# Kernel optimization log

Hardware: AMD Instinct MI355X
Metric: run time of the kernel (lower is better)

The kernel has to match this reference:

```python
import jax, jax.numpy as jnp
import numpy as np

N, S, F, D = 4096, 128, 128, 256  # batch, memory slots, feat_dim, dim_h_o
EPS = 1e-8  # torch CosineSimilarity eps


def _xavier(key, shape):
    fan_out, fan_in = shape
    std = float(np.sqrt(2.0 / (fan_in + fan_out)))
    return jax.random.normal(key, shape, dtype=jnp.float32) * std


def setup_inputs() -> dict:
    key = jax.random.key(0)
    ks = jax.random.split(key, 10)
    return {
        "h_o_prev": jax.random.normal(ks[0], (N, D), dtype=jnp.float32),
        "C": jax.random.normal(ks[1], (N, S, F), dtype=jnp.float32),
        "Wk": _xavier(ks[2], (F, D)), "bk": jnp.zeros((F,), jnp.float32),
        "Wb": _xavier(ks[3], (1, D)), "bb": jnp.zeros((1,), jnp.float32),
        "We": _xavier(ks[4], (F, D)), "be": jnp.zeros((F,), jnp.float32),
        "Wv": _xavier(ks[5], (F, D)), "bv": jnp.zeros((F,), jnp.float32),
        "Wih": _xavier(ks[6], (3 * D, F)), "Whh": _xavier(ks[7], (3 * D, D)),
        "bih": jnp.zeros((3 * D,), jnp.float32), "bhh": jnp.zeros((3 * D,), jnp.float32),
    }


def reference(h_o_prev, C, Wk, bk, Wb, bb, We, be, Wv, bv, Wih, Whh, bih, bhh):
    # --- Attention (content addressing) ---
    k = h_o_prev @ Wk.T + bk                              # [N, F]
    beta_pre = h_o_prev @ Wb.T + bb                       # [N, 1]
    # clamp-split softplus trick in source == softplus(x) + 1
    beta = jax.nn.softplus(beta_pre) + 1.0                # [N, 1]
    C_norm = jnp.maximum(jnp.linalg.norm(C, axis=2), EPS)           # [N, S]
    k_norm = jnp.maximum(jnp.linalg.norm(k, axis=1, keepdims=True), EPS)  # [N, 1]
    s = jnp.einsum("nsf,nf->ns", C, k) / (C_norm * k_norm)          # cosine sim [N, S]
    w = jax.nn.softmax(s * beta, axis=1)                  # [N, S]
    # --- Read memory ---
    r = jnp.einsum("ns,nsf->nf", w, C)                    # [N, F]
    # --- GRU cell update (torch GRUCell semantics) ---
    gi = r @ Wih.T + bih                                  # [N, 3D]
    gh = h_o_prev @ Whh.T + bhh                           # [N, 3D]
    i_r, i_z, i_n = jnp.split(gi, 3, axis=1)
    h_r, h_z, h_n = jnp.split(gh, 3, axis=1)
    rg = jax.nn.sigmoid(i_r + h_r)
    z = jax.nn.sigmoid(i_z + h_z)
    n = jnp.tanh(i_n + rg * h_n)
    h_o = (1.0 - z) * n + z * h_o_prev                    # [N, D]
    # --- Write memory (erase + add, outer products) ---
    e = jax.nn.sigmoid(h_o @ We.T + be)                   # [N, F]
    v = h_o @ Wv.T + bv                                   # [N, F]
    w2 = w[:, :, None]                                    # [N, S, 1]
    C_new = C * (1.0 - w2 * e[:, None, :]) + w2 * v[:, None, :]
    return h_o, C_new, k, r
```

## Files before the change

### kernel.cpp

```cpp
#include <hip/hip_runtime.h>
#include <hip/hip_bf16.h>
#include <cstddef>
#include <cstdint>

constexpr int Nn = 4096;
constexpr int Ss = 128;
constexpr int Ff = 128;
constexpr int Dd = 256;
constexpr float EPSV = 1e-8f;

constexpr size_t HO_OFF = 0;
constexpr size_t C_OFF  = (size_t)Nn * Dd;
constexpr size_t K_OFF  = C_OFF + (size_t)Nn * Ss * Ff;
constexpr size_t R_OFF  = K_OFF + (size_t)Nn * Ff;

typedef __attribute__((ext_vector_type(4))) float f4v;
typedef __attribute__((ext_vector_type(8))) short bh8;
typedef __attribute__((ext_vector_type(4))) short bh4;

constexpr int WK_O  = 0;
constexpr int WHH_O = 32768;
constexpr int WIH_O = 229376;
constexpr int WEV_O = 327680;
constexpr int W_TOT = 393216;

__device__ __forceinline__ float sigmf(float x) { return 1.0f / (1.0f + __expf(-x)); }

__device__ __forceinline__ short f2bf(float x) {
    __hip_bfloat16 h = __float2bfloat16(x);
    return *reinterpret_cast<short*>(&h);
}

__device__ __forceinline__ int swzH(int row, int kb) { return row * 512 + (kb ^ ((row & 7) << 4)); }
__device__ __forceinline__ int swzR(int row, int kb) { return row * 256 + (kb ^ ((row & 7) << 4)); }

__device__ __forceinline__ f4v mfma16(bh8 a, bh8 b, f4v c) {
    return __builtin_amdgcn_mfma_f32_16x16x32_bf16(a, b, c, 0, 0, 0);
}

__global__ __launch_bounds__(256) void prep_weights(
    const float* __restrict__ Wk, const float* __restrict__ Whh,
    const float* __restrict__ Wih, const float* __restrict__ We,
    const float* __restrict__ Wv, short* __restrict__ out)
{
    int id = blockIdx.x * 256 + threadIdx.x;
    float v;
    if      (id < WHH_O) v = Wk[id - WK_O];
    else if (id < WIH_O) v = Whh[id - WHH_O];
    else if (id < WEV_O) v = Wih[id - WIH_O];
    else if (id < WEV_O + 32768) v = We[id - WEV_O];
    else v = Wv[id - WEV_O - 32768];
    out[id] = f2bf(v);
}

__global__ __launch_bounds__(512, 6) void mega_kernel(
    const float* __restrict__ C, const float* __restrict__ h_prev,
    const short* __restrict__ WB,
    const float* __restrict__ Wb, const float* __restrict__ bb,
    const float* __restrict__ bk, const float* __restrict__ bhh,
    const float* __restrict__ bih, const float* __restrict__ be,
    const float* __restrict__ bv,
    float* __restrict__ ho, float* __restrict__ Cnew,
    float* __restrict__ kout, float* __restrict__ rout)
{
    __shared__ float sH[8][256];
    __shared__ __align__(16) short sHb[16 * 256];
    __shared__ __align__(16) short sRb[16 * 128];
    __shared__ float sK[8][128];
    __shared__ float sSc[8][128];
    __shared__ float sEV[8][256];

    const int t  = threadIdx.x;
    const int l  = t & 63;
    const int wv = t >> 6;
    const int nb = blockIdx.x * 8;
    char* hb = (char*)sHb;
    char* rb = (char*)sRb;

    const short* WkB  = WB + WK_O;
    const short* WhhB = WB + WHH_O;
    const short* WihB = WB + WIH_O;
    const short* WevB = WB + WEV_O;

    {
        const int f = t * 4, row = f >> 8, col = f & 255;
        float4 hv = *(const float4*)(h_prev + (size_t)(nb + row) * Dd + col);
        *(float4*)&sH[row][col] = hv;
        bh4 hb4 = { f2bf(hv.x), f2bf(hv.y), f2bf(hv.z), f2bf(hv.w) };
        *(bh4*)(hb + swzH(row, col * 2)) = hb4;
        *(int64_t*)(hb + 4096 + t * 8) = 0;
        *(int*)(rb + 2048 + t * 4) = 0;
    }
    __syncthreads();

    {
        const int fr = l & 15, kq = l >> 4, rbase = kq * 4;
        const int colg = wv * 16 + fr;
        f4v acc = {0.f, 0.f, 0.f, 0.f};
#pragma unroll
        for (int kc = 0; kc < 8; ++kc) {
            bh8 a = *(const bh8*)(hb + swzH(fr, kc * 64 + kq * 16));
            bh8 b = *(const bh8*)(WkB + (size_t)colg * 256 + kc * 32 + kq * 8);
            acc = mfma16(a, b, acc);
        }
        if (rbase < 8) {
            const float bs = bk[colg];
#pragma unroll
            for (int rg = 0; rg < 4; ++rg) {
                float x = acc[rg] + bs;
                sK[rbase + rg][colg] = x;
                kout[(size_t)(nb + rbase + rg) * Ff + colg] = x;
            }
        }
    }
    __syncthreads();

    float invL_r = 0.0f;
    {
        const int half = l >> 5, fl = l & 31, f4 = fl * 4;
        const float* Cn = C + (size_t)(nb + wv) * (Ss * Ff);

        float kv0 = sK[wv][l], kv1 = sK[wv][64 + l];
        float ks = kv0 * kv0 + kv1 * kv1;
#pragma unroll
        for (int o = 32; o > 0; o >>= 1) ks += __shfl_xor(ks, o);
        const float knorm = fmaxf(sqrtf(ks), EPSV);

        float4 hv = *(const float4*)&sH[wv][l * 4];
        float4 wb4 = *(const float4*)(Wb + l * 4);
        float bp = hv.x * wb4.x + hv.y * wb4.y + hv.z * wb4.z + hv.w * wb4.w;
#pragma unroll
        for (int o = 32; o > 0; o >>= 1) bp += __shfl_xor(bp, o);
        bp += bb[0];
        const float beta = ((bp > 20.0f) ? bp : log1pf(__expf(bp))) + 1.0f;

        const float4 kreg = *(const float4*)&sK[wv][f4];
        float lsum = 0.0f;
        f4v racc = {0.f, 0.f, 0.f, 0.f};

#pragma unroll 4
        for (int k = 0; k < 64; ++k) {
            const int s = k * 2 + half;
            const f4v c4 = *(const f4v*)(Cn + (size_t)s * Ff + f4);
            float d = c4.x * kreg.x + c4.y * kreg.y + c4.z * kreg.z + c4.w * kreg.w;
            float q = c4.x * c4.x + c4.y * c4.y + c4.z * c4.z + c4.w * c4.w;
#pragma unroll
            for (int o = 16; o > 0; o >>= 1) {
                d += __shfl_xor(d, o);
                q += __shfl_xor(q, o);
            }
            const float cn = fmaxf(sqrtf(q), EPSV);
            const float x = d / (cn * knorm) * beta;
            const float p = __expf(x - beta);
            if (fl == 0) sSc[wv][s] = p;
            lsum += p;
            racc += p * c4;
        }
        const float L = lsum + __shfl_xor(lsum, 32);
        f4v r2;
        r2.x = __shfl_xor(racc.x, 32); r2.y = __shfl_xor(racc.y, 32);
        r2.z = __shfl_xor(racc.z, 32); r2.w = __shfl_xor(racc.w, 32);
        const float iL = 1.0f / L;
        f4v r4 = (racc + r2) * iL;
        if (half == 0) {
            *(f4v*)(rout + (size_t)(nb + wv) * Ff + f4) = r4;
            bh4 rb4 = { f2bf(r4.x), f2bf(r4.y), f2bf(r4.z), f2bf(r4.w) };
            *(bh4*)(rb + swzR(wv, f4 * 2)) = rb4;
        }
        invL_r = iL;
    }
    __syncthreads();

    {
        const int fr = l & 15, kq = l >> 4, rbase = kq * 4;
        float hoReg[2][4];
#pragma unroll
        for (int dp = 0; dp < 2; ++dp) {
            f4v aG[3], aI[3];
#pragma unroll
            for (int gi = 0; gi < 3; ++gi) {
                const int colg = (gi * 2 + dp) * 128 + wv * 16 + fr;
                f4v g = {0.f, 0.f, 0.f, 0.f}, ii = {0.f, 0.f, 0.f, 0.f};
#pragma unroll
                for (int kc = 0; kc < 8; ++kc) {
                    bh8 a = *(const bh8*)(hb + swzH(fr, kc * 64 + kq * 16));
                    bh8 b = *(const bh8*)(WhhB + (size_t)colg * 256 + kc * 32 + kq * 8);
                    g = mfma16(a, b, g);
                }
#pragma unroll
                for (int kc = 0; kc < 4; ++kc) {
                    bh8 a = *(const bh8*)(rb + swzR(fr, kc * 64 + kq * 16));
                    bh8 b = *(const bh8*)(WihB + (size_t)colg * 128 + kc * 32 + kq * 8);
                    ii = mfma16(a, b, ii);
                }
                aG[gi] = g; aI[gi] = ii;
            }
            if (rbase < 8) {
                const int d = dp * 128 + wv * 16 + fr;
                const float br  = bhh[d] + bih[d];
                const float bz  = bhh[256 + d] + bih[256 + d];
                const float bhn = bhh[512 + d];
                const float bin = bih[512 + d];
#pragma unroll
                for (int rg = 0; rg < 4; ++rg) {
                    const float rgt = sigmf(aG[0][rg] + aI[0][rg] + br);
                    const float z   = sigmf(aG[1][rg] + aI[1][rg] + bz);
                    const float nn  = tanhf(aI[2][rg] + bin + rgt * (aG[2][rg] + bhn));
                    const float hp  = sH[rbase + rg][d];
                    hoReg[dp][rg] = (1.0f - z) * nn + z * hp;
                }
            }
        }
        __syncthreads();
        if (rbase < 8) {
#pragma unroll
            for (int dp = 0; dp < 2; ++dp) {
                const int d = dp * 128 + wv * 16 + fr;
#pragma unroll
                for (int rg = 0; rg < 4; ++rg) {
                    const int row = rbase + rg;
                    const float o = hoReg[dp][rg];
                    ho[(size_t)(nb + row) * Dd + d] = o;
                    *(short*)(hb + row * 512 + ((d * 2) ^ ((row & 7) << 4))) = f2bf(o);
                }
            }
        }
    }
    __syncthreads();

    {
        const int fr = l & 15, kq = l >> 4, rbase = kq * 4;
#pragma unroll
        for (int i = 0; i < 2; ++i) {
            const int colg = i * 128 + wv * 16 + fr;
            f4v acc = {0.f, 0.f, 0.f, 0.f};
#pragma unroll
            for (int kc = 0; kc < 8; ++kc) {
                bh8 a = *(const bh8*)(hb + swzH(fr, kc * 64 + kq * 16));
                bh8 b = *(const bh8*)(WevB + (size_t)colg * 256 + kc * 32 + kq * 8);
                acc = mfma16(a, b, acc);
            }
            if (rbase < 8) {
                const float bs = (colg < 128) ? be[colg] : bv[colg - 128];
#pragma unroll
                for (int rg = 0; rg < 4; ++rg) {
                    float x = acc[rg] + bs;
                    if (colg < 128) x = sigmf(x);
                    sEV[rbase + rg][colg] = x;
                }
            }
        }
    }
    __syncthreads();

    {
        const int half = l >> 5, fl = l & 31, f4 = fl * 4;
        const float* Cn = C    + (size_t)(nb + wv) * (Ss * Ff);
        float*       Co = Cnew + (size_t)(nb + wv) * (Ss * Ff);
        const f4v e4 = *(const f4v*)&sEV[wv][f4];
        const f4v v4 = *(const f4v*)&sEV[wv][128 + f4];
        const float iL = invL_r;

#pragma unroll 4
        for (int k = 0; k < 64; ++k) {
            const int s = k * 2 + half;
            const f4v c4 = *(const f4v*)(Cn + (size_t)s * Ff + f4);
            const float wsc = sSc[wv][s] * iL;
            f4v o = c4 * (1.0f - wsc * e4) + wsc * v4;
            __builtin_nontemporal_store(o, (f4v*)(Co + (size_t)s * Ff + f4));
        }
    }
}

extern "C" void kernel_launch(void* const* d_in, const int* in_sizes, int n_in,
                              void* d_out, int out_size, void* d_ws, size_t ws_size,
                              hipStream_t stream)
{
    const float* h_prev = (const float*)d_in[0];
    const float* C      = (const float*)d_in[1];
    const float* Wk     = (const float*)d_in[2];
    const float* bk     = (const float*)d_in[3];
    const float* Wb     = (const float*)d_in[4];
    const float* bb     = (const float*)d_in[5];
    const float* We     = (const float*)d_in[6];
    const float* be     = (const float*)d_in[7];
    const float* Wv     = (const float*)d_in[8];
    const float* bv     = (const float*)d_in[9];
    const float* Wih    = (const float*)d_in[10];
    const float* Whh    = (const float*)d_in[11];
    const float* bih    = (const float*)d_in[12];
    const float* bhh    = (const float*)d_in[13];

    float* out  = (float*)d_out;
    float* ho   = out + HO_OFF;
    float* Cnew = out + C_OFF;
    float* kbuf = out + K_OFF;
    float* rbuf = out + R_OFF;

    short* wsB = (short*)d_ws;

    prep_weights<<<W_TOT / 256, 256, 0, stream>>>(Wk, Whh, Wih, We, Wv, wsB);

    mega_kernel<<<Nn / 8, 512, 0, stream>>>(
        C, h_prev, wsB, Wb, bb, bk, bhh, bih, be, bv,
        ho, Cnew, kbuf, rbuf);
}
```

Before: 221.1 us.

## Compute per-slot cosine scores per lane to drop shuffle reductions

The attention score pass now gives each lane whole memory rows (slots l and l+64) and accumulates dot products and squared norms serially over the feature dimension, so the per-slot cross-lane shuffle reductions go away. A second pass rereads C with the original coalesced layout to accumulate the weighted read vector, using scores taken from shared memory. This trades shuffle and reduction latency for an uncoalesced strided read pattern and a second pass over C (likely L2/L1 hits). Launch bounds are loosened from 6 to 4 waves per SIMD to give the compiler more registers.

```diff
diff --git a/kernel.cpp b/kernel.cpp
--- a/kernel.cpp
+++ b/kernel.cpp
@@ -53,7 +53,7 @@
     out[id] = f2bf(v);
 }
 
-__global__ __launch_bounds__(512, 6) void mega_kernel(
+__global__ __launch_bounds__(512, 4) void mega_kernel(
     const float* __restrict__ C, const float* __restrict__ h_prev,
     const short* __restrict__ WB,
     const float* __restrict__ Wb, const float* __restrict__ bb,
@@ -117,7 +117,6 @@
 
     float invL_r = 0.0f;
     {
-        const int half = l >> 5, fl = l & 31, f4 = fl * 4;
         const float* Cn = C + (size_t)(nb + wv) * (Ss * Ff);
 
         float kv0 = sK[wv][l], kv1 = sK[wv][64 + l];
@@ -134,40 +133,49 @@
         bp += bb[0];
         const float beta = ((bp > 20.0f) ? bp : log1pf(__expf(bp))) + 1.0f;
 
-        const float4 kreg = *(const float4*)&sK[wv][f4];
-        float lsum = 0.0f;
+        const float* rowA = Cn + (size_t)l * Ff;
+        const float* rowB = rowA + 64 * Ff;
+        float dA = 0.f, qA = 0.f, dB = 0.f, qB = 0.f;
+#pragma unroll 4
+        for (int fc = 0; fc < 32; ++fc) {
+            const f4v k4 = *(const f4v*)&sK[wv][fc * 4];
+            const f4v a4 = *(const f4v*)(rowA + fc * 4);
+            const f4v b4 = *(const f4v*)(rowB + fc * 4);
+            dA += a4.x * k4.x + a4.y * k4.y + a4.z * k4.z + a4.w * k4.w;
+            qA += a4.x * a4.x + a4.y * a4.y + a4.z * a4.z + a4.w * a4.w;
+            dB += b4.x * k4.x + b4.y * k4.y + b4.z * k4.z + b4.w * k4.w;
+            qB += b4.x * b4.x + b4.y * b4.y + b4.z * b4.z + b4.w * b4.w;
+        }
+        const float xA = dA / (fmaxf(sqrtf(qA), EPSV) * knorm) * beta;
+        const float xB = dB / (fmaxf(sqrtf(qB), EPSV) * knorm) * beta;
+        const float pA = __expf(xA - beta);
+        const float pB = __expf(xB - beta);
+        sSc[wv][l]      = pA;
+        sSc[wv][64 + l] = pB;
+        float lsum = pA + pB;
+#pragma unroll
+        for (int o = 32; o > 0; o >>= 1) lsum += __shfl_xor(lsum, o);
+        const float iL = 1.0f / lsum;
+        invL_r = iL;
+
+        const int half = l >> 5, fl = l & 31, f4 = fl * 4;
         f4v racc = {0.f, 0.f, 0.f, 0.f};
-
 #pragma unroll 4
         for (int k = 0; k < 64; ++k) {
             const int s = k * 2 + half;
+            const float p = sSc[wv][s];
             const f4v c4 = *(const f4v*)(Cn + (size_t)s * Ff + f4);
-            float d = c4.x * kreg.x + c4.y * kreg.y + c4.z * kreg.z + c4.w * kreg.w;
-            float q = c4.x * c4.x + c4.y * c4.y + c4.z * c4.z + c4.w * c4.w;
-#pragma unroll
-            for (int o = 16; o > 0; o >>= 1) {
-                d += __shfl_xor(d, o);
-                q += __shfl_xor(q, o);
-            }
-            const float cn = fmaxf(sqrtf(q), EPSV);
-            const float x = d / (cn * knorm) * beta;
-            const float p = __expf(x - beta);
-            if (fl == 0) sSc[wv][s] = p;
-            lsum += p;
             racc += p * c4;
         }
-        const float L = lsum + __shfl_xor(lsum, 32);
         f4v r2;
         r2.x = __shfl_xor(racc.x, 32); r2.y = __shfl_xor(racc.y, 32);
         r2.z = __shfl_xor(racc.z, 32); r2.w = __shfl_xor(racc.w, 32);
-        const float iL = 1.0f / L;
         f4v r4 = (racc + r2) * iL;
         if (half == 0) {
             *(f4v*)(rout + (size_t)(nb + wv) * Ff + f4) = r4;
             bh4 rb4 = { f2bf(r4.x), f2bf(r4.y), f2bf(r4.z), f2bf(r4.w) };
             *(bh4*)(rb + swzR(wv, f4 * 2)) = rb4;
         }
-        invL_r = iL;
     }
     __syncthreads();
 
```

Result: no change. 220.3 us (-0.4%).

## Restructure attention scoring into 16-row tiles with 4-lane reductions

Applied to the files above, without the earlier changes.

Scoring now gives each group of 4 lanes one memory row, so 16 rows are scored per tile. The dot and norm reductions shrink from 5 shuffle steps per row to 2, and beta/knorm is folded into one multiplier. The read accumulation runs as a second pass that reads C again and takes the probabilities from shared memory; it relies on a single wavefront writing and then reading sSc without a barrier. The launch-bounds occupancy hint also drops from 6 to 4, which gives the compiler more registers but allows fewer resident waves.

```diff
diff --git a/kernel.cpp b/kernel.cpp
--- a/kernel.cpp
+++ b/kernel.cpp
@@ -53,7 +53,7 @@
     out[id] = f2bf(v);
 }
 
-__global__ __launch_bounds__(512, 6) void mega_kernel(
+__global__ __launch_bounds__(512, 4) void mega_kernel(
     const float* __restrict__ C, const float* __restrict__ h_prev,
     const short* __restrict__ WB,
     const float* __restrict__ Wb, const float* __restrict__ bb,
@@ -117,7 +117,6 @@
 
     float invL_r = 0.0f;
     {
-        const int half = l >> 5, fl = l & 31, f4 = fl * 4;
         const float* Cn = C + (size_t)(nb + wv) * (Ss * Ff);
 
         float kv0 = sK[wv][l], kv1 = sK[wv][64 + l];
@@ -133,41 +132,54 @@
         for (int o = 32; o > 0; o >>= 1) bp += __shfl_xor(bp, o);
         bp += bb[0];
         const float beta = ((bp > 20.0f) ? bp : log1pf(__expf(bp))) + 1.0f;
-
-        const float4 kreg = *(const float4*)&sK[wv][f4];
+        const float bOkn = beta / knorm;
+
+        const int qrow = l >> 2;
+        const int subf = l & 3;
+        const int half = l >> 5, fl = l & 31, f4 = fl * 4;
         float lsum = 0.0f;
         f4v racc = {0.f, 0.f, 0.f, 0.f};
 
-#pragma unroll 4
-        for (int k = 0; k < 64; ++k) {
-            const int s = k * 2 + half;
-            const f4v c4 = *(const f4v*)(Cn + (size_t)s * Ff + f4);
-            float d = c4.x * kreg.x + c4.y * kreg.y + c4.z * kreg.z + c4.w * kreg.w;
-            float q = c4.x * c4.x + c4.y * c4.y + c4.z * c4.z + c4.w * c4.w;
-#pragma unroll
-            for (int o = 16; o > 0; o >>= 1) {
-                d += __shfl_xor(d, o);
-                q += __shfl_xor(q, o);
-            }
-            const float cn = fmaxf(sqrtf(q), EPSV);
-            const float x = d / (cn * knorm) * beta;
+#pragma unroll 1
+        for (int tile = 0; tile < 8; ++tile) {
+            const int s0 = tile * 16;
+            const float* rowp = Cn + (size_t)(s0 + qrow) * Ff + subf * 32;
+            float d = 0.f, q = 0.f;
+#pragma unroll
+            for (int fc = 0; fc < 8; ++fc) {
+                const f4v c4 = *(const f4v*)(rowp + fc * 4);
+                const f4v k4 = *(const f4v*)&sK[wv][subf * 32 + fc * 4];
+                d += c4.x * k4.x + c4.y * k4.y + c4.z * k4.z + c4.w * k4.w;
+                q += c4.x * c4.x + c4.y * c4.y + c4.z * c4.z + c4.w * c4.w;
+            }
+            d += __shfl_xor(d, 1); d += __shfl_xor(d, 2);
+            q += __shfl_xor(q, 1); q += __shfl_xor(q, 2);
+            const float x = d / fmaxf(sqrtf(q), EPSV) * bOkn;
             const float p = __expf(x - beta);
-            if (fl == 0) sSc[wv][s] = p;
+            if (subf == 0) sSc[wv][s0 + qrow] = p;
             lsum += p;
-            racc += p * c4;
-        }
-        const float L = lsum + __shfl_xor(lsum, 32);
+#pragma unroll
+            for (int j = 0; j < 8; ++j) {
+                const int s = s0 + j * 2 + half;
+                const float pp = sSc[wv][s];
+                const f4v c4 = *(const f4v*)(Cn + (size_t)s * Ff + f4);
+                racc += pp * c4;
+            }
+        }
+#pragma unroll
+        for (int o = 32; o > 0; o >>= 1) lsum += __shfl_xor(lsum, o);
+        const float iL = 4.0f / lsum;
+        invL_r = iL;
+
         f4v r2;
         r2.x = __shfl_xor(racc.x, 32); r2.y = __shfl_xor(racc.y, 32);
         r2.z = __shfl_xor(racc.z, 32); r2.w = __shfl_xor(racc.w, 32);
-        const float iL = 1.0f / L;
         f4v r4 = (racc + r2) * iL;
         if (half == 0) {
             *(f4v*)(rout + (size_t)(nb + wv) * Ff + f4) = r4;
             bh4 rb4 = { f2bf(r4.x), f2bf(r4.y), f2bf(r4.z), f2bf(r4.w) };
             *(bh4*)(rb + swzR(wv, f4 * 2)) = rb4;
         }
-        invL_r = iL;
     }
     __syncthreads();
 
```

Result: faster. 192.9 us (-12.8%).
